# Kernel tuning notes

Hardware: AMD Instinct MI355X
Metric: run time of the kernel (lower is better)

Reference implementation:

```python
import jax, jax.numpy as jnp
import numpy as np

# config matching init_kwargs
SW_SIZE = 512       # signal_window_size
SUBW = 256          # subwindow_size
NSW = 2             # subwindow_nbins = time_points // subwindow_size
DCT_NBINS = 8
NDCT = SUBW // DCT_NBINS   # 32, also nfreqs
NF = 64             # dct_num_filters
SLOPE = 0.02        # LeakyReLU negative slope
HW = 8


def dct2_mat(N):
    # torch_dct.dct with norm=None: X_k = 2 * sum_n x_n cos(pi*(2n+1)*k/(2N))
    n = jnp.arange(N, dtype=jnp.float32)
    k = jnp.arange(N, dtype=jnp.float32)
    return 2.0 * jnp.cos(jnp.pi * (2.0 * n[None, :] + 1.0) * k[:, None] / (2.0 * N))


def setup_inputs() -> dict:
    key = jax.random.key(0)
    k1, k2, k3 = jax.random.split(key, 3)
    x = jax.random.normal(k1, (1024, 1, SW_SIZE, HW, HW), dtype=jnp.float32)
    W = jax.random.normal(k2, (NSW, NF, NDCT, HW, HW), dtype=jnp.float32) * 0.02
    b = jax.random.normal(k3, (NSW, NF), dtype=jnp.float32) * 0.02
    return {"x": x, "W": W, "b": b}


def reference(x, W, b):
    B = x.shape[0]
    # time_slice_interval=1 and maxpool=1 are identity.
    # split time into (subwindows, dct bins, ndct points): [B, NSW, DCT_NBINS, NDCT, 8, 8]
    xs = x[:, 0].reshape(B, NSW, DCT_NBINS, NDCT, HW, HW)
    Ct = dct2_mat(NDCT)
    Cs = dct2_mat(HW)
    # dct_3d: DCT-II along last three dims (time-in-bin, H, W)
    y = jnp.einsum('ft,bsctij->bscfij', Ct, xs)
    y = jnp.einsum('pi,bscfij->bscfpj', Cs, y)
    y = jnp.einsum('qj,bscfpj->bscfpq', Cs, y)
    # mean over dct bins -> [B, NSW, NDCT, 8, 8]
    m = jnp.mean(y, axis=2)
    # per-subwindow full-receptive-field Conv3d == dot product -> [B, NSW, NF]
    feat = jnp.einsum('bsfpq,sofpq->bso', m, W) + b[None, :, :]
    # dropout is identity (eval / rate 0); LeakyReLU then flatten from dim 1
    feat = jnp.where(feat >= 0, feat, SLOPE * feat)
    return feat.reshape(B, -1)
```

## Files before the change

kernel.cpp:

```cpp
#include <hip/hip_runtime.h>

#define NSW 2
#define NDCT 32
#define NF 64
#define KDIM 2048
#define SLOPE 0.02f
#define PI_F 3.14159265358979323846f

__global__ __launch_bounds__(256) void veff_kernel(const float* __restrict__ W,
                                                   float* __restrict__ Veff) {
    __shared__ float Ct[32][32];
    __shared__ float Cs[8][8];
    __shared__ float bufA[2048];
    __shared__ float bufB[2048];
    const int tid = threadIdx.x;

    for (int idx = tid; idx < 1024; idx += 256) {
        int f = idx >> 5, t = idx & 31;
        Ct[f][t] = 2.0f * cosf(PI_F * (float)((2 * t + 1) * f) * (1.0f / 64.0f));
    }
    if (tid < 64) {
        int p = tid >> 3, i = tid & 7;
        Cs[p][i] = 2.0f * cosf(PI_F * (float)((2 * i + 1) * p) * (1.0f / 16.0f));
    }
    const float* Wso = W + blockIdx.x * 2048;
    for (int idx = tid; idx < 2048; idx += 256) bufA[idx] = Wso[idx];
    __syncthreads();

    for (int idx = tid; idx < 2048; idx += 256) {
        int t = idx >> 6, pq = idx & 63;
        float s = 0.f;
        #pragma unroll
        for (int f = 0; f < 32; ++f) s += Ct[f][t] * bufA[f * 64 + pq];
        bufB[idx] = s;
    }
    __syncthreads();
    for (int idx = tid; idx < 2048; idx += 256) {
        int t = idx >> 6, i = (idx >> 3) & 7, q = idx & 7;
        float s = 0.f;
        #pragma unroll
        for (int p = 0; p < 8; ++p) s += Cs[p][i] * bufB[t * 64 + p * 8 + q];
        bufA[idx] = s;
    }
    __syncthreads();
    for (int idx = tid; idx < 2048; idx += 256) {
        int t = idx >> 6, i = (idx >> 3) & 7, j = idx & 7;
        float s = 0.f;
        #pragma unroll
        for (int q = 0; q < 8; ++q) s += Cs[q][j] * bufA[t * 64 + i * 8 + q];
        Veff[blockIdx.x * 2048 + idx] = 0.125f * s;
    }
}

__global__ __launch_bounds__(256) void fused_kernel(const float* __restrict__ x,
                                                    const float* __restrict__ Veff,
                                                    const float* __restrict__ bias,
                                                    float* __restrict__ out) {
    __shared__ float4 Xs4[4 * 512];
    __shared__ float4 Vs4[64 * 33];
    __shared__ float  part[4][4][64];
    const int s   = blockIdx.y;
    const int b0  = blockIdx.x * 4;
    const int tid = threadIdx.x;

    const float4* xbase = (const float4*)x;
    #pragma unroll
    for (int b = 0; b < 4; ++b) {
        #pragma unroll
        for (int r = 0; r < 2; ++r) {
            int k4 = tid + r * 256;
            const float4* xp = xbase + (((size_t)(b0 + b) * 512 + s * 256) * 16 + k4);
            float4 acc = make_float4(0.f, 0.f, 0.f, 0.f);
            #pragma unroll
            for (int c = 0; c < 8; ++c) {
                float4 v = xp[c * 512];
                acc.x += v.x; acc.y += v.y; acc.z += v.z; acc.w += v.w;
            }
            Xs4[b * 512 + k4] = acc;
        }
    }

    const int o  = tid & 63;
    const int kq = tid >> 6;
    const float4* Veff4 = (const float4*)Veff + (size_t)s * 64 * 512;

    float acc0 = 0.f, acc1 = 0.f, acc2 = 0.f, acc3 = 0.f;
    for (int kt = 0; kt < 16; ++kt) {
        __syncthreads();
        #pragma unroll
        for (int j = 0; j < 8; ++j) {
            int idx = tid + j * 256;
            int oo = idx >> 5, k4 = idx & 31;
            Vs4[oo * 33 + k4] = Veff4[oo * 512 + kt * 32 + k4];
        }
        __syncthreads();
        #pragma unroll
        for (int m = 0; m < 8; ++m) {
            int k4 = kq * 8 + m;
            float4 v  = Vs4[o * 33 + k4];
            float4 x0 = Xs4[0 * 512 + kt * 32 + k4];
            float4 x1 = Xs4[1 * 512 + kt * 32 + k4];
            float4 x2 = Xs4[2 * 512 + kt * 32 + k4];
            float4 x3 = Xs4[3 * 512 + kt * 32 + k4];
            acc0 += v.x * x0.x + v.y * x0.y + v.z * x0.z + v.w * x0.w;
            acc1 += v.x * x1.x + v.y * x1.y + v.z * x1.z + v.w * x1.w;
            acc2 += v.x * x2.x + v.y * x2.y + v.z * x2.z + v.w * x2.w;
            acc3 += v.x * x3.x + v.y * x3.y + v.z * x3.z + v.w * x3.w;
        }
    }

    part[kq][0][o] = acc0;
    part[kq][1][o] = acc1;
    part[kq][2][o] = acc2;
    part[kq][3][o] = acc3;
    __syncthreads();
    {
        int b = tid >> 6, oo = tid & 63;
        float f = part[0][b][oo] + part[1][b][oo] + part[2][b][oo] + part[3][b][oo]
                + bias[s * 64 + oo];
        f = (f >= 0.f) ? f : SLOPE * f;
        out[(size_t)(b0 + b) * 128 + s * 64 + oo] = f;
    }
}

extern "C" void kernel_launch(void* const* d_in, const int* in_sizes, int n_in,
                              void* d_out, int out_size, void* d_ws, size_t ws_size,
                              hipStream_t stream) {
    const float* x    = (const float*)d_in[0];
    const float* W    = (const float*)d_in[1];
    const float* bias = (const float*)d_in[2];
    float* out = (float*)d_out;

    const int B = in_sizes[0] / (512 * 64);

    float* Veff = (float*)d_ws;

    veff_kernel<<<NSW * NF, 256, 0, stream>>>(W, Veff);
    fused_kernel<<<dim3(B / 4, NSW), 256, 0, stream>>>(x, Veff, bias, out);
}
```

Measured before the change: 219.6 us.

## Split fused kernel into transpose-sum, split-K GEMM and epilogue kernels

Replaces the single fused bin-sum plus dot-product kernel with three kernels. The first sums the DCT bins and writes the result transposed; the second is a split-K register-blocked GEMM over the transposed weights; the third reduces the partial sums and applies bias and LeakyReLU. This is meant to remove the poor reuse of the effective weights (each 4-batch block reloaded all of them) and raise parallelism, at the cost of extra global round trips, a larger workspace and more launches.

Measured after the change: 227.3 us. +3.5%, slower.

```diff
diff --git a/kernel.cpp b/kernel.cpp
--- a/kernel.cpp
+++ b/kernel.cpp
@@ -8,7 +8,7 @@
 #define PI_F 3.14159265358979323846f
 
 __global__ __launch_bounds__(256) void veff_kernel(const float* __restrict__ W,
-                                                   float* __restrict__ Veff) {
+                                                   float* __restrict__ VeffT) {
     __shared__ float Ct[32][32];
     __shared__ float Cs[8][8];
     __shared__ float bufA[2048];
@@ -29,98 +29,114 @@
 
     for (int idx = tid; idx < 2048; idx += 256) {
         int t = idx >> 6, pq = idx & 63;
-        float s = 0.f;
+        float acc = 0.f;
         #pragma unroll
-        for (int f = 0; f < 32; ++f) s += Ct[f][t] * bufA[f * 64 + pq];
-        bufB[idx] = s;
+        for (int f = 0; f < 32; ++f) acc += Ct[f][t] * bufA[f * 64 + pq];
+        bufB[idx] = acc;
     }
     __syncthreads();
     for (int idx = tid; idx < 2048; idx += 256) {
         int t = idx >> 6, i = (idx >> 3) & 7, q = idx & 7;
-        float s = 0.f;
+        float acc = 0.f;
         #pragma unroll
-        for (int p = 0; p < 8; ++p) s += Cs[p][i] * bufB[t * 64 + p * 8 + q];
-        bufA[idx] = s;
+        for (int p = 0; p < 8; ++p) acc += Cs[p][i] * bufB[t * 64 + p * 8 + q];
+        bufA[idx] = acc;
     }
     __syncthreads();
+    const int so_s = blockIdx.x >> 6;
+    const int so_o = blockIdx.x & 63;
     for (int idx = tid; idx < 2048; idx += 256) {
         int t = idx >> 6, i = (idx >> 3) & 7, j = idx & 7;
-        float s = 0.f;
+        float acc = 0.f;
         #pragma unroll
-        for (int q = 0; q < 8; ++q) s += Cs[q][j] * bufA[t * 64 + i * 8 + q];
-        Veff[blockIdx.x * 2048 + idx] = 0.125f * s;
+        for (int q = 0; q < 8; ++q) acc += Cs[q][j] * bufA[t * 64 + i * 8 + q];
+        VeffT[((size_t)so_s * KDIM + idx) * NF + so_o] = 0.125f * acc;
     }
 }
 
-__global__ __launch_bounds__(256) void fused_kernel(const float* __restrict__ x,
-                                                    const float* __restrict__ Veff,
-                                                    const float* __restrict__ bias,
-                                                    float* __restrict__ out) {
-    __shared__ float4 Xs4[4 * 512];
-    __shared__ float4 Vs4[64 * 33];
-    __shared__ float  part[4][4][64];
-    const int s   = blockIdx.y;
-    const int b0  = blockIdx.x * 4;
+__global__ __launch_bounds__(256) void csumT_kernel(const float* __restrict__ x,
+                                                    float* __restrict__ xsumT,
+                                                    int B) {
+    __shared__ float Xt[256 * 33];
+    const int bt  = blockIdx.x;
+    const int kc  = blockIdx.y;
+    const int s   = blockIdx.z;
     const int tid = threadIdx.x;
+    const int lane = tid & 63;
+    const int w    = tid >> 6;
 
-    const float4* xbase = (const float4*)x;
+    const float4* x4 = (const float4*)x;
     #pragma unroll
-    for (int b = 0; b < 4; ++b) {
+    for (int bi = 0; bi < 8; ++bi) {
+        const int b_local = w * 8 + bi;
+        size_t base = ((size_t)(bt * 32 + b_local) * 512 + s * 256 + kc * 4) * 16 + lane;
+        float4 a = make_float4(0.f, 0.f, 0.f, 0.f);
         #pragma unroll
-        for (int r = 0; r < 2; ++r) {
-            int k4 = tid + r * 256;
-            const float4* xp = xbase + (((size_t)(b0 + b) * 512 + s * 256) * 16 + k4);
-            float4 acc = make_float4(0.f, 0.f, 0.f, 0.f);
-            #pragma unroll
-            for (int c = 0; c < 8; ++c) {
-                float4 v = xp[c * 512];
-                acc.x += v.x; acc.y += v.y; acc.z += v.z; acc.w += v.w;
-            }
-            Xs4[b * 512 + k4] = acc;
+        for (int c = 0; c < 8; ++c) {
+            float4 v = x4[base + (size_t)c * 512];
+            a.x += v.x; a.y += v.y; a.z += v.z; a.w += v.w;
         }
+        float* p = &Xt[lane * 132 + b_local];
+        p[0] = a.x; p[33] = a.y; p[66] = a.z; p[99] = a.w;
+    }
+    __syncthreads();
+
+    const int b  = tid & 31;
+    const int kk = tid >> 5;
+    float* dst = xsumT + ((size_t)s * KDIM + kc * 256) * B + bt * 32 + b;
+    #pragma unroll
+    for (int pass = 0; pass < 32; ++pass) {
+        int k = pass * 8 + kk;
+        dst[(size_t)k * B] = Xt[k * 33 + b];
+    }
+}
+
+__global__ __launch_bounds__(256) void gemm_kernel(const float* __restrict__ xsumT,
+                                                   const float* __restrict__ VeffT,
+                                                   float* __restrict__ part,
+                                                   int B) {
+    const int bt   = blockIdx.x;
+    const int ky   = blockIdx.y;
+    const int s    = blockIdx.z;
+    const int lane = threadIdx.x & 63;
+    const int og   = __builtin_amdgcn_readfirstlane(threadIdx.x >> 6);
+
+    const float* xp = xsumT + ((size_t)s * KDIM + ky * 128) * B + bt * 64 + lane;
+    const float* wp = VeffT + ((size_t)s * KDIM + ky * 128) * NF + og * 16;
+
+    float acc[16];
+    #pragma unroll
+    for (int i = 0; i < 16; ++i) acc[i] = 0.f;
+
+    #pragma unroll 4
+    for (int k = 0; k < 128; ++k) {
+        float xv = xp[(size_t)k * B];
+        const float4* w4 = (const float4*)(wp + (size_t)k * NF);
+        float4 w0 = w4[0], w1 = w4[1], w2 = w4[2], w3 = w4[3];
+        acc[0]  += w0.x * xv; acc[1]  += w0.y * xv; acc[2]  += w0.z * xv; acc[3]  += w0.w * xv;
+        acc[4]  += w1.x * xv; acc[5]  += w1.y * xv; acc[6]  += w1.z * xv; acc[7]  += w1.w * xv;
+        acc[8]  += w2.x * xv; acc[9]  += w2.y * xv; acc[10] += w2.z * xv; acc[11] += w2.w * xv;
+        acc[12] += w3.x * xv; acc[13] += w3.y * xv; acc[14] += w3.z * xv; acc[15] += w3.w * xv;
     }
 
-    const int o  = tid & 63;
-    const int kq = tid >> 6;
-    const float4* Veff4 = (const float4*)Veff + (size_t)s * 64 * 512;
+    float* pp = part + ((size_t)ky * 128 + s * 64 + og * 16) * B + bt * 64 + lane;
+    #pragma unroll
+    for (int o = 0; o < 16; ++o) pp[(size_t)o * B] = acc[o];
+}
 
-    float acc0 = 0.f, acc1 = 0.f, acc2 = 0.f, acc3 = 0.f;
-    for (int kt = 0; kt < 16; ++kt) {
-        __syncthreads();
-        #pragma unroll
-        for (int j = 0; j < 8; ++j) {
-            int idx = tid + j * 256;
-            int oo = idx >> 5, k4 = idx & 31;
-            Vs4[oo * 33 + k4] = Veff4[oo * 512 + kt * 32 + k4];
-        }
-        __syncthreads();
-        #pragma unroll
-        for (int m = 0; m < 8; ++m) {
-            int k4 = kq * 8 + m;
-            float4 v  = Vs4[o * 33 + k4];
-            float4 x0 = Xs4[0 * 512 + kt * 32 + k4];
-            float4 x1 = Xs4[1 * 512 + kt * 32 + k4];
-            float4 x2 = Xs4[2 * 512 + kt * 32 + k4];
-            float4 x3 = Xs4[3 * 512 + kt * 32 + k4];
-            acc0 += v.x * x0.x + v.y * x0.y + v.z * x0.z + v.w * x0.w;
-            acc1 += v.x * x1.x + v.y * x1.y + v.z * x1.z + v.w * x1.w;
-            acc2 += v.x * x2.x + v.y * x2.y + v.z * x2.z + v.w * x2.w;
-            acc3 += v.x * x3.x + v.y * x3.y + v.z * x3.z + v.w * x3.w;
-        }
-    }
-
-    part[kq][0][o] = acc0;
-    part[kq][1][o] = acc1;
-    part[kq][2][o] = acc2;
-    part[kq][3][o] = acc3;
-    __syncthreads();
-    {
-        int b = tid >> 6, oo = tid & 63;
-        float f = part[0][b][oo] + part[1][b][oo] + part[2][b][oo] + part[3][b][oo]
-                + bias[s * 64 + oo];
-        f = (f >= 0.f) ? f : SLOPE * f;
-        out[(size_t)(b0 + b) * 128 + s * 64 + oo] = f;
-    }
+__global__ __launch_bounds__(256) void epi_kernel(const float* __restrict__ part,
+                                                  const float* __restrict__ bias,
+                                                  float* __restrict__ out,
+                                                  int B) {
+    const int g  = blockIdx.x * 256 + threadIdx.x;
+    const int b  = g & (B - 1);
+    const int so = g / B;
+    float sum = bias[so];
+    #pragma unroll
+    for (int ky = 0; ky < 16; ++ky)
+        sum += part[((size_t)ky * 128 + so) * B + b];
+    sum = (sum >= 0.f) ? sum : SLOPE * sum;
+    out[(size_t)b * 128 + so] = sum;
 }
 
 extern "C" void kernel_launch(void* const* d_in, const int* in_sizes, int n_in,
@@ -133,8 +149,12 @@
 
     const int B = in_sizes[0] / (512 * 64);
 
-    float* Veff = (float*)d_ws;
+    float* VeffT = (float*)d_ws;
+    float* xsumT = VeffT + (size_t)NSW * KDIM * NF;
+    float* part  = xsumT + (size_t)NSW * KDIM * B;
 
-    veff_kernel<<<NSW * NF, 256, 0, stream>>>(W, Veff);
-    fused_kernel<<<dim3(B / 4, NSW), 256, 0, stream>>>(x, Veff, bias, out);
+    veff_kernel<<<NSW * NF, 256, 0, stream>>>(W, VeffT);
+    csumT_kernel<<<dim3(B / 32, 8, NSW), 256, 0, stream>>>(x, xsumT, B);
+    gemm_kernel<<<dim3(B / 64, 16, NSW), 256, 0, stream>>>(xsumT, VeffT, part, B);
+    epi_kernel<<<(B * 128) / 256, 256, 0, stream>>>(part, bias, out, B);
 }
```

## Transpose Veff layout and stream weights directly from global memory

Applied to the files above, without the earlier changes.

The Veff kernel now writes the effective weights interleaved by output channel in float4 groups, so adjacent threads read adjacent float4s. The fused kernel drops the shared-memory staging of weight tiles and its per-tile barriers, and each thread streams its slice of weights straight from global or L2 memory. This removes many __syncthreads and LDS traffic, but relies on cache hits for weights reused across all blocks.

Measured after the change: 213.0 us. 1.03x faster.

```diff
diff --git a/kernel.cpp b/kernel.cpp
--- a/kernel.cpp
+++ b/kernel.cpp
@@ -29,35 +29,37 @@
 
     for (int idx = tid; idx < 2048; idx += 256) {
         int t = idx >> 6, pq = idx & 63;
-        float s = 0.f;
+        float acc = 0.f;
         #pragma unroll
-        for (int f = 0; f < 32; ++f) s += Ct[f][t] * bufA[f * 64 + pq];
-        bufB[idx] = s;
+        for (int f = 0; f < 32; ++f) acc += Ct[f][t] * bufA[f * 64 + pq];
+        bufB[idx] = acc;
     }
     __syncthreads();
     for (int idx = tid; idx < 2048; idx += 256) {
         int t = idx >> 6, i = (idx >> 3) & 7, q = idx & 7;
-        float s = 0.f;
+        float acc = 0.f;
         #pragma unroll
-        for (int p = 0; p < 8; ++p) s += Cs[p][i] * bufB[t * 64 + p * 8 + q];
-        bufA[idx] = s;
+        for (int p = 0; p < 8; ++p) acc += Cs[p][i] * bufB[t * 64 + p * 8 + q];
+        bufA[idx] = acc;
     }
     __syncthreads();
+    const int so_s = blockIdx.x >> 6;
+    const int so_o = blockIdx.x & 63;
     for (int idx = tid; idx < 2048; idx += 256) {
         int t = idx >> 6, i = (idx >> 3) & 7, j = idx & 7;
-        float s = 0.f;
+        float acc = 0.f;
         #pragma unroll
-        for (int q = 0; q < 8; ++q) s += Cs[q][j] * bufA[t * 64 + i * 8 + q];
-        Veff[blockIdx.x * 2048 + idx] = 0.125f * s;
+        for (int q = 0; q < 8; ++q) acc += Cs[q][j] * bufA[t * 64 + i * 8 + q];
+        Veff[(((size_t)so_s * 512 + (idx >> 2)) * 64 + so_o) * 4 + (idx & 3)] =
+            0.125f * acc;
     }
 }
 
-__global__ __launch_bounds__(256) void fused_kernel(const float* __restrict__ x,
-                                                    const float* __restrict__ Veff,
-                                                    const float* __restrict__ bias,
-                                                    float* __restrict__ out) {
+__global__ __launch_bounds__(256) void fused2_kernel(const float* __restrict__ x,
+                                                     const float* __restrict__ Veff,
+                                                     const float* __restrict__ bias,
+                                                     float* __restrict__ out) {
     __shared__ float4 Xs4[4 * 512];
-    __shared__ float4 Vs4[64 * 33];
     __shared__ float  part[4][4][64];
     const int s   = blockIdx.y;
     const int b0  = blockIdx.x * 4;
@@ -79,34 +81,25 @@
             Xs4[b * 512 + k4] = acc;
         }
     }
+    __syncthreads();
 
     const int o  = tid & 63;
     const int kq = tid >> 6;
-    const float4* Veff4 = (const float4*)Veff + (size_t)s * 64 * 512;
+    const float4* wp = (const float4*)Veff + ((size_t)s * 512 + kq * 128) * 64 + o;
+    const float4* xq = Xs4 + kq * 128;
 
     float acc0 = 0.f, acc1 = 0.f, acc2 = 0.f, acc3 = 0.f;
-    for (int kt = 0; kt < 16; ++kt) {
-        __syncthreads();
-        #pragma unroll
-        for (int j = 0; j < 8; ++j) {
-            int idx = tid + j * 256;
-            int oo = idx >> 5, k4 = idx & 31;
-            Vs4[oo * 33 + k4] = Veff4[oo * 512 + kt * 32 + k4];
-        }
-        __syncthreads();
-        #pragma unroll
-        for (int m = 0; m < 8; ++m) {
-            int k4 = kq * 8 + m;
-            float4 v  = Vs4[o * 33 + k4];
-            float4 x0 = Xs4[0 * 512 + kt * 32 + k4];
-            float4 x1 = Xs4[1 * 512 + kt * 32 + k4];
-            float4 x2 = Xs4[2 * 512 + kt * 32 + k4];
-            float4 x3 = Xs4[3 * 512 + kt * 32 + k4];
-            acc0 += v.x * x0.x + v.y * x0.y + v.z * x0.z + v.w * x0.w;
-            acc1 += v.x * x1.x + v.y * x1.y + v.z * x1.z + v.w * x1.w;
-            acc2 += v.x * x2.x + v.y * x2.y + v.z * x2.z + v.w * x2.w;
-            acc3 += v.x * x3.x + v.y * x3.y + v.z * x3.z + v.w * x3.w;
-        }
+    #pragma unroll 4
+    for (int m = 0; m < 128; ++m) {
+        float4 w  = wp[(size_t)m * 64];
+        float4 x0 = xq[0 * 512 + m];
+        float4 x1 = xq[1 * 512 + m];
+        float4 x2 = xq[2 * 512 + m];
+        float4 x3 = xq[3 * 512 + m];
+        acc0 += w.x * x0.x + w.y * x0.y + w.z * x0.z + w.w * x0.w;
+        acc1 += w.x * x1.x + w.y * x1.y + w.z * x1.z + w.w * x1.w;
+        acc2 += w.x * x2.x + w.y * x2.y + w.z * x2.z + w.w * x2.w;
+        acc3 += w.x * x3.x + w.y * x3.y + w.z * x3.z + w.w * x3.w;
     }
 
     part[kq][0][o] = acc0;
@@ -136,5 +129,5 @@
     float* Veff = (float*)d_ws;
 
     veff_kernel<<<NSW * NF, 256, 0, stream>>>(W, Veff);
-    fused_kernel<<<dim3(B / 4, NSW), 256, 0, stream>>>(x, Veff, bias, out);
+    fused2_kernel<<<dim3(B / 4, NSW), 256, 0, stream>>>(x, Veff, bias, out);
 }
```
